# Optimization experiments

Measured on AMD Instinct MI355X. Metric: run time of the kernel, lower is better.

Reference implementation:

```python
import jax, jax.numpy as jnp
import numpy as np

N_NODES = 50000
N_EDGES = 800000
LATENT = 32
NODE_IN = 6
EDGE_IN = 3
STEPS = 10
OUT_DIM = 1
NEG_SLOPE = 0.01
LN_EPS = 1e-5


def _leaky(x):
    return jnp.where(x >= 0, x, NEG_SLOPE * x)


def _layernorm(x, scale, bias):
    mu = jnp.mean(x, axis=-1, keepdims=True)
    var = jnp.mean(jnp.square(x - mu), axis=-1, keepdims=True)
    return (x - mu) * jax.lax.rsqrt(var + LN_EPS) * scale + bias


def setup_inputs() -> dict:
    key = jax.random.key(0)
    ks = jax.random.split(key, 24)
    g = lambda i, shape, fan_in: (jax.random.normal(ks[i], shape, jnp.float32)
                                  / np.sqrt(fan_in)).astype(jnp.float32)
    return {
        "x": jax.random.normal(ks[0], (N_NODES, NODE_IN), jnp.float32),
        "edge_attr": jax.random.normal(ks[1], (N_EDGES, EDGE_IN), jnp.float32),
        "senders": jax.random.randint(ks[2], (N_EDGES,), 0, N_NODES, jnp.int32),
        "receivers": jax.random.randint(ks[3], (N_EDGES,), 0, N_NODES, jnp.int32),
        # input embedders (Linear + LeakyReLU)
        "node_enc_W": g(4, (NODE_IN, LATENT), NODE_IN),
        "node_enc_b": jnp.zeros((LATENT,), jnp.float32),
        "edge_enc_W": g(5, (EDGE_IN, LATENT), EDGE_IN),
        "edge_enc_b": jnp.zeros((LATENT,), jnp.float32),
        # per-step edge update: concat(e, x_src, x_dst) -> latent
        "edge_W": g(6, (STEPS, 3 * LATENT, LATENT), 3 * LATENT),
        "edge_b": jnp.zeros((STEPS, LATENT), jnp.float32),
        "edge_ln_scale": jnp.ones((STEPS, LATENT), jnp.float32),
        "edge_ln_bias": jnp.zeros((STEPS, LATENT), jnp.float32),
        # per-step node update: concat(x, agg) -> latent
        "node_W": g(7, (STEPS, 2 * LATENT, LATENT), 2 * LATENT),
        "node_b": jnp.zeros((STEPS, LATENT), jnp.float32),
        "node_ln_scale": jnp.ones((STEPS, LATENT), jnp.float32),
        "node_ln_bias": jnp.zeros((STEPS, LATENT), jnp.float32),
        # decoder
        "dec_W1": g(8, (LATENT, LATENT), LATENT),
        "dec_b1": jnp.zeros((LATENT,), jnp.float32),
        "dec_W2": g(9, (LATENT, OUT_DIM), LATENT),
        "dec_b2": jnp.zeros((OUT_DIM,), jnp.float32),
    }


def _forward(x, edge_attr, senders, receivers,
             node_enc_W, node_enc_b, edge_enc_W, edge_enc_b,
             edge_W, edge_b, edge_ln_scale, edge_ln_bias,
             node_W, node_b, node_ln_scale, node_ln_bias,
             dec_W1, dec_b1, dec_W2, dec_b2):
    n = x.shape[0]
    # encode raw features into latent space
    h = _leaky(x @ node_enc_W + node_enc_b)            # [N, L]
    e = _leaky(edge_attr @ edge_enc_W + edge_enc_b)    # [E, L]
    # receiver in-degree for scatter-mean (constant across steps)
    cnt = jax.ops.segment_sum(jnp.ones((e.shape[0],), e.dtype), receivers,
                              num_segments=n)
    inv_cnt = (1.0 / jnp.maximum(cnt, 1.0))[:, None]   # [N, 1]

    def step(carry, p):
        h, e = carry
        eW, eb, es, ebi, nW, nb, ns, nbi = p
        # edge update: MLP(concat(e, h_src, h_dst)) + inner LN + residual
        m = jnp.concatenate([e, h[senders], h[receivers]], axis=-1)  # [E, 3L]
        m = _layernorm(_leaky(m @ eW + eb), es, ebi)
        e = e + m
        # node update: scatter-mean over receivers, MLP + inner LN + residual
        agg = jax.ops.segment_sum(e, receivers, num_segments=n) * inv_cnt
        u = jnp.concatenate([h, agg], axis=-1)                       # [N, 2L]
        u = _layernorm(_leaky(u @ nW + nb), ns, nbi)
        h = h + u
        return (h, e), None

    (h, e), _ = jax.lax.scan(step, (h, e),
                             (edge_W, edge_b, edge_ln_scale, edge_ln_bias,
                              node_W, node_b, node_ln_scale, node_ln_bias))
    # decoder: Linear -> LeakyReLU -> Linear
    return _leaky(h @ dec_W1 + dec_b1) @ dec_W2 + dec_b2  # [N, 1]


def reference(x, edge_attr, senders, receivers,
              node_enc_W, node_enc_b, edge_enc_W, edge_enc_b,
              edge_W, edge_b, edge_ln_scale, edge_ln_bias,
              node_W, node_b, node_ln_scale, node_ln_bias,
              dec_W1, dec_b1, dec_W2, dec_b2):
    return _forward(x, edge_attr, senders, receivers,
                    node_enc_W, node_enc_b, edge_enc_W, edge_enc_b,
                    edge_W, edge_b, edge_ln_scale, edge_ln_bias,
                    node_W, node_b, node_ln_scale, node_ln_bias,
                    dec_W1, dec_b1, dec_W2, dec_b2)
```

## Files before the change

kernel.cpp:

```cpp
#include <hip/hip_runtime.h>
#include <hip/hip_bf16.h>

#define N_NODES 50000
#define N_EDGES 800000
#define LATENT 32
#define STEPS 10
#define NEG_SLOPE 0.01f
#define LN_EPS 1e-5f
#define SCAN_BLK 256
#define SCAN_NBLK ((N_NODES + SCAN_BLK - 1) / SCAN_BLK)
#define STG_STRIDE 36
#define NODES_PER_BLOCK 64
#define STEP_BLOCKS ((N_NODES + NODES_PER_BLOCK - 1) / NODES_PER_BLOCK)
#define CPAD 65

typedef __attribute__((ext_vector_type(8))) __bf16 bf16x8;
typedef __attribute__((ext_vector_type(4))) __bf16 bf16x4;
typedef __attribute__((ext_vector_type(4))) float f32x4;

__device__ __forceinline__ float leaky(float x) {
    return x >= 0.0f ? x : NEG_SLOPE * x;
}

__device__ __forceinline__ float4 f4fma(float a, float4 b, float4 c) {
    c.x += a * b.x; c.y += a * b.y; c.z += a * b.z; c.w += a * b.w;
    return c;
}

__device__ __forceinline__ bf16x4 pack4(float4 v) {
    bf16x4 o;
    o[0] = (__bf16)v.x; o[1] = (__bf16)v.y; o[2] = (__bf16)v.z; o[3] = (__bf16)v.w;
    return o;
}


__global__ void encode_nodes_kernel(const float* __restrict__ x,
                                    const float* __restrict__ W,
                                    const float* __restrict__ b,
                                    float* __restrict__ h,
                                    __bf16* __restrict__ hbf) {
    __shared__ __align__(16) float Ws[6 * 32];
    __shared__ __align__(16) float bs[32];
    int tid = threadIdx.x;
    if (tid < 192) Ws[tid] = W[tid];
    if (tid < 32) bs[tid] = b[tid];
    __syncthreads();
    int n = blockIdx.x * blockDim.x + tid;
    if (n >= N_NODES) return;
    float xv[6];
#pragma unroll
    for (int k = 0; k < 6; k++) xv[k] = x[(size_t)n * 6 + k];
    float4 acc[8];
#pragma unroll
    for (int q = 0; q < 8; q++) acc[q] = *(const float4*)&bs[q * 4];
#pragma unroll
    for (int k = 0; k < 6; k++) {
#pragma unroll
        for (int q = 0; q < 8; q++) {
            float4 w = *(const float4*)&Ws[k * 32 + q * 4];
            acc[q] = f4fma(xv[k], w, acc[q]);
        }
    }
#pragma unroll
    for (int q = 0; q < 8; q++) {
        float4 o = acc[q];
        o.x = leaky(o.x); o.y = leaky(o.y); o.z = leaky(o.z); o.w = leaky(o.w);
        *(float4*)&h[(size_t)n * 32 + q * 4] = o;
        *(bf16x4*)&hbf[(size_t)n * 32 + q * 4] = pack4(o);
    }
}


__global__ void count_kernel(const int* __restrict__ recv, int* __restrict__ cnt) {
    int i = blockIdx.x * blockDim.x + threadIdx.x;
    if (i < N_EDGES) atomicAdd(&cnt[recv[i]], 1);
}

__global__ void csr_reduce_kernel(const int* __restrict__ cnt, int* __restrict__ partial) {
    __shared__ int sdata[SCAN_BLK];
    int tid = threadIdx.x;
    int idx = blockIdx.x * SCAN_BLK + tid;
    sdata[tid] = (idx < N_NODES) ? cnt[idx] : 0;
    __syncthreads();
#pragma unroll
    for (int off = SCAN_BLK / 2; off > 0; off >>= 1) {
        if (tid < off) sdata[tid] += sdata[tid + off];
        __syncthreads();
    }
    if (tid == 0) partial[blockIdx.x] = sdata[0];
}

__global__ void csr_scan_partials_kernel(int* __restrict__ partial,
                                         int* __restrict__ row_start) {
    __shared__ int sdata[SCAN_BLK];
    int tid = threadIdx.x;
    int v = (tid < SCAN_NBLK) ? partial[tid] : 0;
    sdata[tid] = v;
    __syncthreads();
#pragma unroll
    for (int off = 1; off < SCAN_BLK; off <<= 1) {
        int t = (tid >= off) ? sdata[tid - off] : 0;
        __syncthreads();
        sdata[tid] += t;
        __syncthreads();
    }
    if (tid < SCAN_NBLK) partial[tid] = sdata[tid] - v;
    if (tid == SCAN_BLK - 1) row_start[N_NODES] = sdata[SCAN_BLK - 1];
}

__global__ void csr_apply_kernel(const int* __restrict__ cnt,
                                 const int* __restrict__ partial,
                                 int* __restrict__ row_start,
                                 int* __restrict__ cursor) {
    __shared__ int sdata[SCAN_BLK];
    int tid = threadIdx.x;
    int idx = blockIdx.x * SCAN_BLK + tid;
    int v = (idx < N_NODES) ? cnt[idx] : 0;
    sdata[tid] = v;
    __syncthreads();
#pragma unroll
    for (int off = 1; off < SCAN_BLK; off <<= 1) {
        int t = (tid >= off) ? sdata[tid - off] : 0;
        __syncthreads();
        sdata[tid] += t;
        __syncthreads();
    }
    if (idx < N_NODES) {
        int out = partial[blockIdx.x] + sdata[tid] - v;
        row_start[idx] = out;
        cursor[idx] = out;
    }
}

__global__ void scatter_encode_kernel(const float* __restrict__ ea,
                                      const int* __restrict__ senders,
                                      const int* __restrict__ receivers,
                                      int* __restrict__ cursor,
                                      const float* __restrict__ W,
                                      const float* __restrict__ b,
                                      __bf16* __restrict__ e,
                                      unsigned int* __restrict__ sr_p) {
    __shared__ __align__(16) float Ws[3 * 32];
    __shared__ __align__(16) float bs[32];
    int tid = threadIdx.x;
    if (tid < 96) Ws[tid] = W[tid];
    if (tid < 32) bs[tid] = b[tid];
    __syncthreads();
    int i = blockIdx.x * blockDim.x + tid;
    if (i >= N_EDGES) return;
    int s = senders[i];
    int r = receivers[i];
    float xv[3];
#pragma unroll
    for (int k = 0; k < 3; k++) xv[k] = ea[(size_t)i * 3 + k];
    int pos = atomicAdd(&cursor[r], 1);
    float4 acc[8];
#pragma unroll
    for (int q = 0; q < 8; q++) acc[q] = *(const float4*)&bs[q * 4];
#pragma unroll
    for (int k = 0; k < 3; k++) {
#pragma unroll
        for (int q = 0; q < 8; q++) {
            float4 w = *(const float4*)&Ws[k * 32 + q * 4];
            acc[q] = f4fma(xv[k], w, acc[q]);
        }
    }
    __bf16* er = e + (size_t)pos * 32;
#pragma unroll
    for (int q = 0; q < 4; q++) {
        float4 lo = acc[2 * q], hi = acc[2 * q + 1];
        bf16x8 v;
        v[0] = (__bf16)leaky(lo.x); v[1] = (__bf16)leaky(lo.y);
        v[2] = (__bf16)leaky(lo.z); v[3] = (__bf16)leaky(lo.w);
        v[4] = (__bf16)leaky(hi.x); v[5] = (__bf16)leaky(hi.y);
        v[6] = (__bf16)leaky(hi.z); v[7] = (__bf16)leaky(hi.w);
        *(bf16x8*)(er + q * 8) = v;
    }
    sr_p[pos] = (unsigned int)s | ((unsigned int)r << 16);
}


__global__ __launch_bounds__(256) void fused_step_kernel(
    __bf16* __restrict__ e,
    const __bf16* __restrict__ hbf_in,
    __bf16* __restrict__ hbf_out,
    const float* __restrict__ h_in,
    float* __restrict__ h_out,
    const unsigned int* __restrict__ srp,
    const int* __restrict__ row_start,
    const float* __restrict__ eW,
    const float* __restrict__ eb,
    const float* __restrict__ els,
    const float* __restrict__ elb,
    const float* __restrict__ nW,
    const float* __restrict__ nb,
    const float* __restrict__ nls,
    const float* __restrict__ nlb) {
    __shared__ __align__(16) float stg[4][16 * STG_STRIDE];
    __shared__ __align__(16) float Ws[64 * 32];
    __shared__ __align__(16) float cL[NODES_PER_BLOCK * CPAD];
    __shared__ __align__(16) float prm[96];

    int tid = threadIdx.x;
    const int wave = tid >> 6;
    const int lane = tid & 63;
    const int n_ = lane & 15;
    const int quad = lane >> 4;
    const int rr = lane >> 2;
    const int jj = lane & 3;

    {
        const float4* Wg = (const float4*)nW;
        float4* Wl = (float4*)Ws;
        Wl[tid] = Wg[tid];
        Wl[tid + 256] = Wg[tid + 256];
        if (tid < 32) {
            prm[tid] = nb[tid];
            prm[32 + tid] = nls[tid];
            prm[64 + tid] = nlb[tid];
        }
    }

    bf16x8 bfr[3][2];
#pragma unroll
    for (int kc = 0; kc < 3; kc++)
#pragma unroll
        for (int oh = 0; oh < 2; oh++) {
            bf16x8 f;
#pragma unroll
            for (int j = 0; j < 8; j++)
                f[j] = (__bf16)eW[(kc * 32 + quad * 8 + j) * 32 + oh * 16 + n_];
            bfr[kc][oh] = f;
        }
    float bia0 = eb[n_], bia1 = eb[16 + n_];
    float lns8[8], lnb8[8];
    {
        f32x4 sa = *(const f32x4*)&els[jj * 8];
        f32x4 sb = *(const f32x4*)&els[jj * 8 + 4];
        f32x4 ba = *(const f32x4*)&elb[jj * 8];
        f32x4 bb = *(const f32x4*)&elb[jj * 8 + 4];
#pragma unroll
        for (int i = 0; i < 4; i++) {
            lns8[i] = sa[i]; lns8[4 + i] = sb[i];
            lnb8[i] = ba[i]; lnb8[4 + i] = bb[i];
        }
    }

    const int n0 = blockIdx.x * NODES_PER_BLOCK;
    const int nn = min(NODES_PER_BLOCK, N_NODES - n0);
    const int beg = row_start[n0];
    const int end = row_start[n0 + nn];
    const int nt = (end - beg + 15) >> 4;
    float* mystg = stg[wave];

    unsigned int sr_n2 = 0;
    bf16x8 aE{}, aS{}, aR{}, old{};
    if (wave < nt) {
        int jb = beg + wave * 16;
        int ja = min(jb + n_, N_EDGES - 1);
        unsigned int sr_c = srp[ja];
        aE  = *(const bf16x8*)&e[(size_t)ja * 32 + quad * 8];
        aS  = *(const bf16x8*)&hbf_in[(size_t)(sr_c & 0xFFFFu) * 32 + quad * 8];
        aR  = *(const bf16x8*)&hbf_in[(size_t)(sr_c >> 16) * 32 + quad * 8];
        old = *(const bf16x8*)&e[(size_t)min(jb + rr, N_EDGES - 1) * 32 + jj * 8];
        if (wave + 4 < nt)
            sr_n2 = srp[min(beg + (wave + 4) * 16 + n_, N_EDGES - 1)];
    }
    for (int t = wave; t < nt; t += 4) {
        int e0 = beg + t * 16;

        f32x4 acc[2] = {{0.f, 0.f, 0.f, 0.f}, {0.f, 0.f, 0.f, 0.f}};
#pragma unroll
        for (int oh = 0; oh < 2; oh++) {
            acc[oh] = __builtin_amdgcn_mfma_f32_16x16x32_bf16(aE, bfr[0][oh], acc[oh], 0, 0, 0);
            acc[oh] = __builtin_amdgcn_mfma_f32_16x16x32_bf16(aS, bfr[1][oh], acc[oh], 0, 0, 0);
            acc[oh] = __builtin_amdgcn_mfma_f32_16x16x32_bf16(aR, bfr[2][oh], acc[oh], 0, 0, 0);
        }

        bf16x8 aE_n = aE, aS_n = aS, aR_n = aR, old_n = old;
        if (t + 4 < nt) {
            int jb = beg + (t + 4) * 16;
            int ja = min(jb + n_, N_EDGES - 1);
            aE_n  = *(const bf16x8*)&e[(size_t)ja * 32 + quad * 8];
            aS_n  = *(const bf16x8*)&hbf_in[(size_t)(sr_n2 & 0xFFFFu) * 32 + quad * 8];
            aR_n  = *(const bf16x8*)&hbf_in[(size_t)(sr_n2 >> 16) * 32 + quad * 8];
            old_n = *(const bf16x8*)&e[(size_t)min(jb + rr, N_EDGES - 1) * 32 + jj * 8];
            if (t + 8 < nt)
                sr_n2 = srp[min(beg + (t + 8) * 16 + n_, N_EDGES - 1)];
        }

#pragma unroll
        for (int oh = 0; oh < 2; oh++)
#pragma unroll
            for (int g = 0; g < 4; g++)
                mystg[(quad * 4 + g) * STG_STRIDE + oh * 16 + n_] =
                    leaky(acc[oh][g] + (oh ? bia1 : bia0));
        __builtin_amdgcn_wave_barrier();

        f32x4 va = *(const f32x4*)&mystg[rr * STG_STRIDE + jj * 8];
        f32x4 vb = *(const f32x4*)&mystg[rr * STG_STRIDE + jj * 8 + 4];
        float s1 = va[0] + va[1] + va[2] + va[3] + vb[0] + vb[1] + vb[2] + vb[3];
        float s2 = va[0]*va[0] + va[1]*va[1] + va[2]*va[2] + va[3]*va[3]
                 + vb[0]*vb[0] + vb[1]*vb[1] + vb[2]*vb[2] + vb[3]*vb[3];
        s1 += __shfl_xor(s1, 1);  s2 += __shfl_xor(s2, 1);
        s1 += __shfl_xor(s1, 2);  s2 += __shfl_xor(s2, 2);
        float mu = s1 * (1.0f / 32.0f);
        float var = s2 * (1.0f / 32.0f) - mu * mu;
        float inv = rsqrtf(fmaxf(var, 0.0f) + LN_EPS);

        float v[8] = {va[0], va[1], va[2], va[3], vb[0], vb[1], vb[2], vb[3]};
        bf16x8 outp;
#pragma unroll
        for (int i = 0; i < 8; i++)
            outp[i] = (__bf16)((float)old[i] + (v[i] - mu) * inv * lns8[i] + lnb8[i]);
        if (e0 + rr < end)
            *(bf16x8*)&e[(size_t)(e0 + rr) * 32 + jj * 8] = outp;
        __builtin_amdgcn_wave_barrier();

        aE = aE_n; aS = aS_n; aR = aR_n; old = old_n;
    }

    __syncthreads();

    const int nl = tid >> 2;
    const int cq = tid & 3;
    float hreg[8] = {0, 0, 0, 0, 0, 0, 0, 0};
    if (nl < nn) {
        int n = n0 + nl;
        int bn = row_start[n], en = row_start[n + 1];
        float s8[8];
#pragma unroll
        for (int k = 0; k < 8; k++) s8[k] = 0.f;
        int j = bn;
        for (; j + 3 < en; j += 4) {
            bf16x8 v0 = *(const bf16x8*)&e[(size_t)j * 32 + cq * 8];
            bf16x8 v1 = *(const bf16x8*)&e[(size_t)(j + 1) * 32 + cq * 8];
            bf16x8 v2 = *(const bf16x8*)&e[(size_t)(j + 2) * 32 + cq * 8];
            bf16x8 v3 = *(const bf16x8*)&e[(size_t)(j + 3) * 32 + cq * 8];
#pragma unroll
            for (int k = 0; k < 8; k++)
                s8[k] += (float)v0[k] + (float)v1[k] + (float)v2[k] + (float)v3[k];
        }
        for (; j < en; j++) {
            bf16x8 v = *(const bf16x8*)&e[(size_t)j * 32 + cq * 8];
#pragma unroll
            for (int k = 0; k < 8; k++) s8[k] += (float)v[k];
        }
        float ic = 1.0f / fmaxf((float)(en - bn), 1.0f);
        float4 hv0 = *(const float4*)&h_in[(size_t)n * 32 + cq * 8];
        float4 hv1 = *(const float4*)&h_in[(size_t)n * 32 + cq * 8 + 4];
        hreg[0] = hv0.x; hreg[1] = hv0.y; hreg[2] = hv0.z; hreg[3] = hv0.w;
        hreg[4] = hv1.x; hreg[5] = hv1.y; hreg[6] = hv1.z; hreg[7] = hv1.w;
        float* crow = &cL[nl * CPAD];
#pragma unroll
        for (int k = 0; k < 8; k++) {
            crow[cq * 8 + k] = hreg[k];
            crow[32 + cq * 8 + k] = s8[k] * ic;
        }
    }
    __syncthreads();
    if (nl < nn) {
        int n = n0 + nl;
        float4 acc0 = *(const float4*)&prm[cq * 8];
        float4 acc1 = *(const float4*)&prm[cq * 8 + 4];
        const float* crow = &cL[nl * CPAD];
#pragma unroll
        for (int k = 0; k < 64; k++) {
            float ck = crow[k];
            acc0 = f4fma(ck, *(const float4*)&Ws[k * 32 + cq * 8], acc0);
            acc1 = f4fma(ck, *(const float4*)&Ws[k * 32 + cq * 8 + 4], acc1);
        }
        float m8[8] = {leaky(acc0.x), leaky(acc0.y), leaky(acc0.z), leaky(acc0.w),
                       leaky(acc1.x), leaky(acc1.y), leaky(acc1.z), leaky(acc1.w)};
        float s1 = 0.f, s2 = 0.f;
#pragma unroll
        for (int k = 0; k < 8; k++) { s1 += m8[k]; s2 += m8[k] * m8[k]; }
        s1 += __shfl_xor(s1, 1);  s2 += __shfl_xor(s2, 1);
        s1 += __shfl_xor(s1, 2);  s2 += __shfl_xor(s2, 2);
        float mu = s1 * (1.0f / 32.0f);
        float var = s2 * (1.0f / 32.0f) - mu * mu;
        float inv = rsqrtf(fmaxf(var, 0.0f) + LN_EPS);
        float res[8];
#pragma unroll
        for (int k = 0; k < 8; k++)
            res[k] = hreg[k] + (m8[k] - mu) * inv * prm[32 + cq * 8 + k] + prm[64 + cq * 8 + k];
        float4 r0 = {res[0], res[1], res[2], res[3]};
        float4 r1 = {res[4], res[5], res[6], res[7]};
        *(float4*)&h_out[(size_t)n * 32 + cq * 8] = r0;
        *(float4*)&h_out[(size_t)n * 32 + cq * 8 + 4] = r1;
        bf16x8 hb;
#pragma unroll
        for (int k = 0; k < 8; k++) hb[k] = (__bf16)res[k];
        *(bf16x8*)&hbf_out[(size_t)n * 32 + cq * 8] = hb;
    }
}


__global__ void decoder_kernel(const float* __restrict__ h,
                               const float* __restrict__ W1,
                               const float* __restrict__ b1,
                               const float* __restrict__ W2,
                               const float* __restrict__ b2,
                               float* __restrict__ out) {
    __shared__ __align__(16) float W1s[32 * 32];
    __shared__ __align__(16) float prm[65];
    int tid = threadIdx.x;
    {
        const float4* Wg = (const float4*)W1;
        float4* Wl = (float4*)W1s;
        Wl[tid] = Wg[tid];
        if (tid < 32) { prm[tid] = b1[tid]; prm[32 + tid] = W2[tid]; }
        if (tid == 0) prm[64] = b2[0];
    }
    __syncthreads();
    int n = blockIdx.x * blockDim.x + tid;
    if (n >= N_NODES) return;
    float hv[32];
#pragma unroll
    for (int q = 0; q < 8; q++) {
        float4 v = *(const float4*)&h[(size_t)n * 32 + q * 4];
        hv[q * 4 + 0] = v.x; hv[q * 4 + 1] = v.y; hv[q * 4 + 2] = v.z; hv[q * 4 + 3] = v.w;
    }
    float4 acc[8];
#pragma unroll
    for (int q = 0; q < 8; q++) acc[q] = *(const float4*)&prm[q * 4];
#pragma unroll
    for (int k = 0; k < 32; k++) {
#pragma unroll
        for (int q = 0; q < 8; q++) {
            float4 w = *(const float4*)&W1s[k * 32 + q * 4];
            acc[q] = f4fma(hv[k], w, acc[q]);
        }
    }
    float o = prm[64];
#pragma unroll
    for (int q = 0; q < 8; q++) {
        o += leaky(acc[q].x) * prm[32 + q * 4 + 0];
        o += leaky(acc[q].y) * prm[32 + q * 4 + 1];
        o += leaky(acc[q].z) * prm[32 + q * 4 + 2];
        o += leaky(acc[q].w) * prm[32 + q * 4 + 3];
    }
    out[n] = o;
}


extern "C" void kernel_launch(void* const* d_in, const int* in_sizes, int n_in,
                              void* d_out, int out_size, void* d_ws, size_t ws_size,
                              hipStream_t stream) {
    const float* x          = (const float*)d_in[0];
    const float* edge_attr  = (const float*)d_in[1];
    const int*   senders    = (const int*)d_in[2];
    const int*   receivers  = (const int*)d_in[3];
    const float* node_enc_W = (const float*)d_in[4];
    const float* node_enc_b = (const float*)d_in[5];
    const float* edge_enc_W = (const float*)d_in[6];
    const float* edge_enc_b = (const float*)d_in[7];
    const float* edge_W     = (const float*)d_in[8];
    const float* edge_b     = (const float*)d_in[9];
    const float* edge_ln_s  = (const float*)d_in[10];
    const float* edge_ln_b  = (const float*)d_in[11];
    const float* node_W     = (const float*)d_in[12];
    const float* node_b     = (const float*)d_in[13];
    const float* node_ln_s  = (const float*)d_in[14];
    const float* node_ln_b  = (const float*)d_in[15];
    const float* dec_W1     = (const float*)d_in[16];
    const float* dec_b1     = (const float*)d_in[17];
    const float* dec_W2     = (const float*)d_in[18];
    const float* dec_b2     = (const float*)d_in[19];
    float* out = (float*)d_out;

    char* ws = (char*)d_ws;
    size_t off = 0;
    auto alloc = [&](size_t bytes) -> void* {
        void* p = ws + off;
        off = (off + bytes + 255) & ~(size_t)255;
        return p;
    };
    float*        h0        = (float*)alloc((size_t)N_NODES * 32 * 4);
    float*        h1        = (float*)alloc((size_t)N_NODES * 32 * 4);
    __bf16*       hbf0      = (__bf16*)alloc((size_t)N_NODES * 32 * 2);
    __bf16*       hbf1      = (__bf16*)alloc((size_t)N_NODES * 32 * 2);
    __bf16*       e         = (__bf16*)alloc((size_t)N_EDGES * 32 * 2);
    int*          cnt       = (int*)alloc((size_t)N_NODES * 4);
    int*          row_start = (int*)alloc((size_t)(N_NODES + 1) * 4);
    int*          cursor    = (int*)alloc((size_t)N_NODES * 4);
    unsigned int* sr_p      = (unsigned int*)alloc((size_t)N_EDGES * 4);
    int*          partial   = (int*)alloc((size_t)SCAN_BLK * 4);
    (void)ws_size; (void)in_sizes; (void)n_in; (void)out_size;

    hipMemsetAsync(cnt, 0, (size_t)N_NODES * 4, stream);
    encode_nodes_kernel<<<(N_NODES + 255) / 256, 256, 0, stream>>>(x, node_enc_W, node_enc_b, h0, hbf0);
    count_kernel<<<(N_EDGES + 255) / 256, 256, 0, stream>>>(receivers, cnt);
    csr_reduce_kernel<<<SCAN_NBLK, SCAN_BLK, 0, stream>>>(cnt, partial);
    csr_scan_partials_kernel<<<1, SCAN_BLK, 0, stream>>>(partial, row_start);
    csr_apply_kernel<<<SCAN_NBLK, SCAN_BLK, 0, stream>>>(cnt, partial, row_start, cursor);
    scatter_encode_kernel<<<(N_EDGES + 255) / 256, 256, 0, stream>>>(
        edge_attr, senders, receivers, cursor, edge_enc_W, edge_enc_b, e, sr_p);

    float*  hbufs[2]  = {h0, h1};
    __bf16* hbbufs[2] = {hbf0, hbf1};
    for (int s = 0; s < STEPS; s++) {
        int in = s & 1, outb = 1 - in;
        fused_step_kernel<<<STEP_BLOCKS, 256, 0, stream>>>(
            e, hbbufs[in], hbbufs[outb], hbufs[in], hbufs[outb],
            sr_p, row_start,
            edge_W + (size_t)s * 96 * 32, edge_b + s * 32,
            edge_ln_s + s * 32, edge_ln_b + s * 32,
            node_W + (size_t)s * 64 * 32, node_b + s * 32,
            node_ln_s + s * 32, node_ln_b + s * 32);
    }
    decoder_kernel<<<(N_NODES + 255) / 256, 256, 0, stream>>>(h0, dec_W1, dec_b1, dec_W2, dec_b2, out);
}
```

Baseline: 709.6 us.

## Split node MLP across 8 lanes per node with shuffle reduction, drop LDS staging

Halves nodes per block to 32 and assigns 8 lanes per node, each owning 4 input features. Each lane computes partial products for all 32 outputs from the shared weights, and the partials are combined with xor shuffles. This removes the cL shared staging buffer and one __syncthreads, lowering LDS use and likely raising occupancy. The weight tile is stored padded to stride 36. In exchange it adds many shuffles, keeps 32 accumulators live per thread, and doubles the number of blocks, each of which reloads the weights.

```diff
diff --git a/kernel.cpp b/kernel.cpp
--- a/kernel.cpp
+++ b/kernel.cpp
@@ -10,9 +10,9 @@
 #define SCAN_BLK 256
 #define SCAN_NBLK ((N_NODES + SCAN_BLK - 1) / SCAN_BLK)
 #define STG_STRIDE 36
-#define NODES_PER_BLOCK 64
+#define NODES_PER_BLOCK 32
 #define STEP_BLOCKS ((N_NODES + NODES_PER_BLOCK - 1) / NODES_PER_BLOCK)
-#define CPAD 65
+#define WS_STRIDE 36
 
 typedef __attribute__((ext_vector_type(8))) __bf16 bf16x8;
 typedef __attribute__((ext_vector_type(4))) __bf16 bf16x4;
@@ -197,8 +197,7 @@
     const float* __restrict__ nls,
     const float* __restrict__ nlb) {
     __shared__ __align__(16) float stg[4][16 * STG_STRIDE];
-    __shared__ __align__(16) float Ws[64 * 32];
-    __shared__ __align__(16) float cL[NODES_PER_BLOCK * CPAD];
+    __shared__ __align__(16) float Ws[64 * WS_STRIDE];
     __shared__ __align__(16) float prm[96];
 
     int tid = threadIdx.x;
@@ -211,9 +210,12 @@
 
     {
         const float4* Wg = (const float4*)nW;
-        float4* Wl = (float4*)Ws;
-        Wl[tid] = Wg[tid];
-        Wl[tid + 256] = Wg[tid + 256];
+#pragma unroll
+        for (int r = 0; r < 2; r++) {
+            int i4 = tid + r * 256;
+            float4 val = Wg[i4];
+            *(float4*)&Ws[(i4 >> 3) * WS_STRIDE + (i4 & 7) * 4] = val;
+        }
         if (tid < 32) {
             prm[tid] = nb[tid];
             prm[32 + tid] = nls[tid];
@@ -322,76 +324,87 @@
 
     __syncthreads();
 
-    const int nl = tid >> 2;
-    const int cq = tid & 3;
-    float hreg[8] = {0, 0, 0, 0, 0, 0, 0, 0};
-    if (nl < nn) {
-        int n = n0 + nl;
+    const int nl = tid >> 3;
+    const int oc = tid & 7;
+    const bool act = nl < nn;
+    const int n = n0 + nl;
+    float hv4[4] = {0.f, 0.f, 0.f, 0.f};
+    float ag4[4] = {0.f, 0.f, 0.f, 0.f};
+    if (act) {
         int bn = row_start[n], en = row_start[n + 1];
-        float s8[8];
-#pragma unroll
-        for (int k = 0; k < 8; k++) s8[k] = 0.f;
+        float s4[4] = {0.f, 0.f, 0.f, 0.f};
         int j = bn;
         for (; j + 3 < en; j += 4) {
-            bf16x8 v0 = *(const bf16x8*)&e[(size_t)j * 32 + cq * 8];
-            bf16x8 v1 = *(const bf16x8*)&e[(size_t)(j + 1) * 32 + cq * 8];
-            bf16x8 v2 = *(const bf16x8*)&e[(size_t)(j + 2) * 32 + cq * 8];
-            bf16x8 v3 = *(const bf16x8*)&e[(size_t)(j + 3) * 32 + cq * 8];
-#pragma unroll
-            for (int k = 0; k < 8; k++)
-                s8[k] += (float)v0[k] + (float)v1[k] + (float)v2[k] + (float)v3[k];
+            bf16x4 v0 = *(const bf16x4*)&e[(size_t)j * 32 + oc * 4];
+            bf16x4 v1 = *(const bf16x4*)&e[(size_t)(j + 1) * 32 + oc * 4];
+            bf16x4 v2 = *(const bf16x4*)&e[(size_t)(j + 2) * 32 + oc * 4];
+            bf16x4 v3 = *(const bf16x4*)&e[(size_t)(j + 3) * 32 + oc * 4];
+#pragma unroll
+            for (int k = 0; k < 4; k++)
+                s4[k] += (float)v0[k] + (float)v1[k] + (float)v2[k] + (float)v3[k];
         }
         for (; j < en; j++) {
-            bf16x8 v = *(const bf16x8*)&e[(size_t)j * 32 + cq * 8];
-#pragma unroll
-            for (int k = 0; k < 8; k++) s8[k] += (float)v[k];
+            bf16x4 v = *(const bf16x4*)&e[(size_t)j * 32 + oc * 4];
+#pragma unroll
+            for (int k = 0; k < 4; k++) s4[k] += (float)v[k];
         }
         float ic = 1.0f / fmaxf((float)(en - bn), 1.0f);
-        float4 hv0 = *(const float4*)&h_in[(size_t)n * 32 + cq * 8];
-        float4 hv1 = *(const float4*)&h_in[(size_t)n * 32 + cq * 8 + 4];
-        hreg[0] = hv0.x; hreg[1] = hv0.y; hreg[2] = hv0.z; hreg[3] = hv0.w;
-        hreg[4] = hv1.x; hreg[5] = hv1.y; hreg[6] = hv1.z; hreg[7] = hv1.w;
-        float* crow = &cL[nl * CPAD];
-#pragma unroll
-        for (int k = 0; k < 8; k++) {
-            crow[cq * 8 + k] = hreg[k];
-            crow[32 + cq * 8 + k] = s8[k] * ic;
-        }
-    }
-    __syncthreads();
-    if (nl < nn) {
-        int n = n0 + nl;
-        float4 acc0 = *(const float4*)&prm[cq * 8];
-        float4 acc1 = *(const float4*)&prm[cq * 8 + 4];
-        const float* crow = &cL[nl * CPAD];
-#pragma unroll
-        for (int k = 0; k < 64; k++) {
-            float ck = crow[k];
-            acc0 = f4fma(ck, *(const float4*)&Ws[k * 32 + cq * 8], acc0);
-            acc1 = f4fma(ck, *(const float4*)&Ws[k * 32 + cq * 8 + 4], acc1);
-        }
-        float m8[8] = {leaky(acc0.x), leaky(acc0.y), leaky(acc0.z), leaky(acc0.w),
-                       leaky(acc1.x), leaky(acc1.y), leaky(acc1.z), leaky(acc1.w)};
+        float4 hvv = *(const float4*)&h_in[(size_t)n * 32 + oc * 4];
+        hv4[0] = hvv.x; hv4[1] = hvv.y; hv4[2] = hvv.z; hv4[3] = hvv.w;
+#pragma unroll
+        for (int k = 0; k < 4; k++) ag4[k] = s4[k] * ic;
+    }
+
+    float4 acc[8];
+#pragma unroll
+    for (int q = 0; q < 8; q++) acc[q] = {0.f, 0.f, 0.f, 0.f};
+#pragma unroll
+    for (int kk = 0; kk < 4; kk++) {
+        int kh = oc * 4 + kk;
+        int ka = 32 + oc * 4 + kk;
+#pragma unroll
+        for (int q = 0; q < 8; q++) {
+            acc[q] = f4fma(hv4[kk], *(const float4*)&Ws[kh * WS_STRIDE + q * 4], acc[q]);
+            acc[q] = f4fma(ag4[kk], *(const float4*)&Ws[ka * WS_STRIDE + q * 4], acc[q]);
+        }
+    }
+#pragma unroll
+    for (int msk = 1; msk <= 4; msk <<= 1) {
+#pragma unroll
+        for (int q = 0; q < 8; q++) {
+            acc[q].x += __shfl_xor(acc[q].x, msk);
+            acc[q].y += __shfl_xor(acc[q].y, msk);
+            acc[q].z += __shfl_xor(acc[q].z, msk);
+            acc[q].w += __shfl_xor(acc[q].w, msk);
+        }
+    }
+
+    if (act) {
         float s1 = 0.f, s2 = 0.f;
-#pragma unroll
-        for (int k = 0; k < 8; k++) { s1 += m8[k]; s2 += m8[k] * m8[k]; }
-        s1 += __shfl_xor(s1, 1);  s2 += __shfl_xor(s2, 1);
-        s1 += __shfl_xor(s1, 2);  s2 += __shfl_xor(s2, 2);
+        float m_own[4];
+#pragma unroll
+        for (int q = 0; q < 8; q++) {
+            float mq[4] = {leaky(acc[q].x + prm[q * 4 + 0]),
+                           leaky(acc[q].y + prm[q * 4 + 1]),
+                           leaky(acc[q].z + prm[q * 4 + 2]),
+                           leaky(acc[q].w + prm[q * 4 + 3])};
+#pragma unroll
+            for (int k = 0; k < 4; k++) { s1 += mq[k]; s2 += mq[k] * mq[k]; }
+            if (q == oc) {
+#pragma unroll
+                for (int k = 0; k < 4; k++) m_own[k] = mq[k];
+            }
+        }
         float mu = s1 * (1.0f / 32.0f);
         float var = s2 * (1.0f / 32.0f) - mu * mu;
         float inv = rsqrtf(fmaxf(var, 0.0f) + LN_EPS);
-        float res[8];
-#pragma unroll
-        for (int k = 0; k < 8; k++)
-            res[k] = hreg[k] + (m8[k] - mu) * inv * prm[32 + cq * 8 + k] + prm[64 + cq * 8 + k];
+        float res[4];
+#pragma unroll
+        for (int k = 0; k < 4; k++)
+            res[k] = hv4[k] + (m_own[k] - mu) * inv * prm[32 + oc * 4 + k] + prm[64 + oc * 4 + k];
         float4 r0 = {res[0], res[1], res[2], res[3]};
-        float4 r1 = {res[4], res[5], res[6], res[7]};
-        *(float4*)&h_out[(size_t)n * 32 + cq * 8] = r0;
-        *(float4*)&h_out[(size_t)n * 32 + cq * 8 + 4] = r1;
-        bf16x8 hb;
-#pragma unroll
-        for (int k = 0; k < 8; k++) hb[k] = (__bf16)res[k];
-        *(bf16x8*)&hbf_out[(size_t)n * 32 + cq * 8] = hb;
+        *(float4*)&h_out[(size_t)n * 32 + oc * 4] = r0;
+        *(bf16x4*)&hbf_out[(size_t)n * 32 + oc * 4] = pack4(r0);
     }
 }
 
```

Result: no change. 714.9 us (+0.7%).
